# Kernel tuning notes

Hardware: AMD Instinct MI355X
Metric: run time of the kernel (lower is better)

Reference implementation:

```python
import jax, jax.numpy as jnp
import numpy as np


def setup_inputs() -> dict:
    key = jax.random.key(0)
    ks = jax.random.split(key, 5)
    N, D, H, E = 8192, 1024, 4096, 8
    s = 0.02
    return {
        "x": jax.random.normal(ks[0], (N, D), jnp.float32),
        "Wr": jax.random.normal(ks[1], (D, E), jnp.float32) * s,
        "br": jnp.zeros((E,), jnp.float32),
        "W1": jax.random.normal(ks[2], (E, D, H), jnp.float32) * s,
        "b1": jnp.zeros((E, H), jnp.float32),
        "W2": jax.random.normal(ks[3], (E, H, D), jnp.float32) * s,
        "b2": jnp.zeros((E, D), jnp.float32),
        "k": 2,
    }


def reference(x, Wr, br, W1, b1, W2, b2, k):
    # Router (eval mode: no gate noise)
    logits = x @ Wr + br                      # [N, E]
    scores = jax.nn.softmax(logits, axis=-1)  # [N, E]
    topk_vals, topk_inds = jax.lax.top_k(scores, k)  # [N, k]
    N, E = scores.shape
    # dispatch_mask: zeros scattered with top-k probabilities
    dispatch_mask = jnp.zeros_like(scores).at[
        jnp.arange(N)[:, None], topk_inds
    ].set(topk_vals)                          # [N, E]
    # Dense all-expert FFN compute (faithful to the original wasteful pattern)
    h = jax.nn.relu(jnp.einsum('nd,edh->neh', x, W1) + b1)   # [N, E, H]
    expert_outputs = jnp.einsum('neh,ehd->ned', h, W2) + b2  # [N, E, D]
    output = jnp.einsum('ned,ne->nd', expert_outputs, dispatch_mask)  # [N, D]
    # Load-balancing aux loss (torch.var is unbiased, ddof=1)
    importance = dispatch_mask.sum(axis=0)    # [E]
    imp_mean = jnp.mean(importance)
    imp_var = jnp.var(importance, ddof=1)
    aux_loss = imp_var / (imp_mean ** 2 + 1e-9)
    return output, aux_loss
```

## Files before the change

kernel.cpp:

```cpp
#include <hip/hip_runtime.h>
#include <hip/hip_bf16.h>


#define NTOK 8192
#define DDIM 1024
#define HDIM 4096
#define NEXP 8
#define NASSIGN (NTOK * 2)
#define MAX_MTILES 136

typedef __bf16 bf16_t;
typedef __bf16 bf16x8 __attribute__((ext_vector_type(8)));
typedef float f32x4 __attribute__((ext_vector_type(4)));

#define GLOAD16(gptr, lptr)                                                    \
  __builtin_amdgcn_global_load_lds(                                            \
      (const __attribute__((address_space(1))) void*)(gptr),                   \
      (__attribute__((address_space(3))) void*)(lptr), 16, 0, 0)


__global__ void __launch_bounds__(256) cvt_x_kernel(
    const float* __restrict__ in, bf16_t* __restrict__ out) {
  const int i = (blockIdx.x * 256 + threadIdx.x) * 8;
  const float4 a = *(const float4*)(in + i);
  const float4 b = *(const float4*)(in + i + 4);
  bf16x8 o;
  o[0] = (bf16_t)a.x; o[1] = (bf16_t)a.y; o[2] = (bf16_t)a.z; o[3] = (bf16_t)a.w;
  o[4] = (bf16_t)b.x; o[5] = (bf16_t)b.y; o[6] = (bf16_t)b.z; o[7] = (bf16_t)b.w;
  *(bf16x8*)(out + i) = o;
}

__global__ void __launch_bounds__(256) transpose_cvt_kernel(
    const float* __restrict__ in, bf16_t* __restrict__ out, int R, int C) {
  __shared__ float tile[32][33];
  const size_t mat = (size_t)R * C;
  const float* ip = in + (size_t)blockIdx.z * mat;
  bf16_t* op = out + (size_t)blockIdx.z * mat;
  const int c0 = blockIdx.x * 32, r0 = blockIdx.y * 32;
  const int tx = threadIdx.x, ty = threadIdx.y;
#pragma unroll
  for (int i = 0; i < 4; ++i) {
    const int r = ty + 8 * i;
    tile[r][tx] = ip[(size_t)(r0 + r) * C + (c0 + tx)];
  }
  __syncthreads();
#pragma unroll
  for (int i = 0; i < 4; ++i) {
    const int r = ty + 8 * i;
    op[(size_t)(c0 + r) * R + (r0 + tx)] = (bf16_t)tile[tx][r];
  }
}


__global__ void __launch_bounds__(256) router_kernel(
    const float* __restrict__ x, const float* __restrict__ Wr,
    const float* __restrict__ br, int2* __restrict__ ids,
    float2* __restrict__ prs, int* __restrict__ counts) {
  const int n = blockIdx.x;
  const int t = threadIdx.x;
  const float* xr = x + (size_t)n * DDIM;
  float acc[NEXP];
#pragma unroll
  for (int e = 0; e < NEXP; ++e) acc[e] = 0.f;
#pragma unroll
  for (int j = 0; j < DDIM / 256; ++j) {
    const int d = t + 256 * j;
    const float xv = xr[d];
    const float* w = Wr + (size_t)d * NEXP;
#pragma unroll
    for (int e = 0; e < NEXP; ++e) acc[e] += xv * w[e];
  }
  __shared__ float red[256][NEXP];
#pragma unroll
  for (int e = 0; e < NEXP; ++e) red[t][e] = acc[e];
  __syncthreads();
  for (int s = 128; s >= 1; s >>= 1) {
    if (t < s) {
#pragma unroll
      for (int e = 0; e < NEXP; ++e) red[t][e] += red[t + s][e];
    }
    __syncthreads();
  }
  if (t == 0) {
    float l[NEXP];
#pragma unroll
    for (int e = 0; e < NEXP; ++e) l[e] = red[0][e] + br[e];
    int i1 = 0; float v1 = l[0];
    for (int e = 1; e < NEXP; ++e)
      if (l[e] > v1) { v1 = l[e]; i1 = e; }
    int i2 = (i1 == 0) ? 1 : 0; float v2 = l[i2];
    for (int e = 0; e < NEXP; ++e)
      if (e != i1 && l[e] > v2) { v2 = l[e]; i2 = e; }
    float denom = 0.f;
    for (int e = 0; e < NEXP; ++e) denom += expf(l[e] - v1);
    const float p1 = expf(v1 - v1) / denom;
    const float p2 = expf(v2 - v1) / denom;
    ids[n] = make_int2(i1, i2);
    prs[n] = make_float2(p1, p2);
    atomicAdd(&counts[i1], 1);
    atomicAdd(&counts[i2], 1);
  }
}

__global__ void scan_kernel(const int* __restrict__ counts,
                            int* __restrict__ offsets, int* __restrict__ tmap) {
  if (threadIdx.x != 0 || blockIdx.x != 0) return;
  int off = 0, nt = 0;
  for (int e = 0; e < NEXP; ++e) {
    offsets[e] = off;
    const int c = counts[e];
    for (int m0 = 0; m0 < c; m0 += 128) {
      tmap[nt] = e;
      tmap[MAX_MTILES + nt] = m0;
      ++nt;
    }
    off += c;
  }
  offsets[NEXP] = off;
  tmap[2 * MAX_MTILES] = nt;
}

__global__ void __launch_bounds__(256) scatter_kernel(
    const int2* __restrict__ ids, const float2* __restrict__ prs,
    const int* __restrict__ offsets, int* __restrict__ cursor,
    int* __restrict__ btok, float* __restrict__ bprob) {
  const int n = blockIdx.x * 256 + threadIdx.x;
  if (n >= NTOK) return;
  const int2 id = ids[n];
  const float2 pr = prs[n];
  int p = atomicAdd(&cursor[id.x], 1);
  btok[offsets[id.x] + p] = n;
  bprob[offsets[id.x] + p] = pr.x;
  p = atomicAdd(&cursor[id.y], 1);
  btok[offsets[id.y] + p] = n;
  bprob[offsets[id.y] + p] = pr.y;
}

__global__ void __launch_bounds__(256) aux_kernel(
    const int2* __restrict__ ids, const float2* __restrict__ prs,
    float* __restrict__ aux_out) {
  const int t = threadIdx.x;
  float imp[NEXP];
#pragma unroll
  for (int e = 0; e < NEXP; ++e) imp[e] = 0.f;
  for (int n = t; n < NTOK; n += 256) {
    const int2 id = ids[n];
    const float2 pr = prs[n];
#pragma unroll
    for (int e = 0; e < NEXP; ++e)
      imp[e] += (id.x == e ? pr.x : 0.f) + (id.y == e ? pr.y : 0.f);
  }
  __shared__ float red[256][NEXP];
#pragma unroll
  for (int e = 0; e < NEXP; ++e) red[t][e] = imp[e];
  __syncthreads();
  for (int s = 128; s >= 1; s >>= 1) {
    if (t < s) {
#pragma unroll
      for (int e = 0; e < NEXP; ++e) red[t][e] += red[t + s][e];
    }
    __syncthreads();
  }
  if (t == 0) {
    float m = 0.f;
    for (int e = 0; e < NEXP; ++e) m += red[0][e];
    m *= (1.f / NEXP);
    float v = 0.f;
    for (int e = 0; e < NEXP; ++e) {
      const float d = red[0][e] - m;
      v += d * d;
    }
    v *= (1.f / (NEXP - 1));
    aux_out[0] = v / (m * m + 1e-9f);
  }
}


__global__ void __launch_bounds__(256) gemm1_kernel(
    const bf16_t* __restrict__ xb, const bf16_t* __restrict__ W1t,
    const float* __restrict__ b1, const int* __restrict__ btok,
    const int* __restrict__ offsets, const int* __restrict__ counts,
    const int* __restrict__ tmap, bf16_t* __restrict__ h) {
  const int tidx = blockIdx.y;
  if (tidx >= tmap[2 * MAX_MTILES]) return;
  const int e = tmap[tidx];
  const int m0 = tmap[MAX_MTILES + tidx];
  const int cnt = counts[e];
  const int aoff = offsets[e];
  const int n0 = blockIdx.x * 128;

  __shared__ __align__(16) bf16_t Al[128 * 32];
  __shared__ __align__(16) bf16_t Bl[128 * 32];

  const int tid = threadIdx.x;
  const int wave = tid >> 6;
  const int lane = tid & 63;

  const bf16_t* asrc[2];
  const bf16_t* bsrc[2];
#pragma unroll
  for (int j = 0; j < 2; ++j) {
    const int fi = j * 256 + tid;
    const int r = fi >> 2;
    const int kc = (fi & 3) * 8;
    int arow = m0 + r;
    if (arow > cnt - 1) arow = cnt - 1;
    const int tok = btok[aoff + arow];
    asrc[j] = xb + (size_t)tok * DDIM + kc;
    bsrc[j] = W1t + ((size_t)e * HDIM + n0 + r) * DDIM + kc;
  }
  char* AlB = (char*)Al + wave * 1024;
  char* BlB = (char*)Bl + wave * 1024;

  f32x4 acc[4][4];
#pragma unroll
  for (int mt = 0; mt < 4; ++mt)
#pragma unroll
    for (int nt = 0; nt < 4; ++nt) acc[mt][nt] = (f32x4){0.f, 0.f, 0.f, 0.f};

  const int wr = (wave >> 1) * 64;
  const int wc = (wave & 1) * 64;
  const int lrow = lane & 15;
  const int lk = (lane >> 4) * 8;

  for (int k0 = 0; k0 < DDIM; k0 += 32) {
    GLOAD16(asrc[0] + k0, AlB);
    GLOAD16(asrc[1] + k0, AlB + 4096);
    GLOAD16(bsrc[0] + k0, BlB);
    GLOAD16(bsrc[1] + k0, BlB + 4096);
    __syncthreads();
    bf16x8 af[4], bfr[4];
#pragma unroll
    for (int mt = 0; mt < 4; ++mt)
      af[mt] = *(const bf16x8*)&Al[(wr + mt * 16 + lrow) * 32 + lk];
#pragma unroll
    for (int nt = 0; nt < 4; ++nt)
      bfr[nt] = *(const bf16x8*)&Bl[(wc + nt * 16 + lrow) * 32 + lk];
#pragma unroll
    for (int mt = 0; mt < 4; ++mt)
#pragma unroll
      for (int nt = 0; nt < 4; ++nt)
        acc[mt][nt] = __builtin_amdgcn_mfma_f32_16x16x32_bf16(
            af[mt], bfr[nt], acc[mt][nt], 0, 0, 0);
    __syncthreads();
  }

  const int rbase = (lane >> 4) * 4;
  const float* b1e = b1 + (size_t)e * HDIM + n0;
#pragma unroll
  for (int nt = 0; nt < 4; ++nt) {
    const int cl = wc + nt * 16 + lrow;
    const float bb = b1e[cl];
#pragma unroll
    for (int mt = 0; mt < 4; ++mt) {
#pragma unroll
      for (int r = 0; r < 4; ++r) {
        const int grow = wr + mt * 16 + rbase + r;
        if (m0 + grow < cnt)
          h[(size_t)(aoff + m0 + grow) * HDIM + (n0 + cl)] =
              (bf16_t)fmaxf(acc[mt][nt][r] + bb, 0.f);
      }
    }
  }
}

__global__ void __launch_bounds__(256) gemm2_kernel(
    const bf16_t* __restrict__ h, const bf16_t* __restrict__ W2t,
    const float* __restrict__ b2, const int* __restrict__ btok,
    const float* __restrict__ bprob, const int* __restrict__ offsets,
    const int* __restrict__ counts, const int* __restrict__ tmap,
    float* __restrict__ out) {
  const int tidx = blockIdx.y;
  if (tidx >= tmap[2 * MAX_MTILES]) return;
  const int e = tmap[tidx];
  const int m0 = tmap[MAX_MTILES + tidx];
  const int cnt = counts[e];
  const int aoff = offsets[e];
  const int n0 = blockIdx.x * 128;

  __shared__ __align__(16) bf16_t Al[128 * 32];
  __shared__ __align__(16) bf16_t Bl[128 * 32];

  const int tid = threadIdx.x;
  const int wave = tid >> 6;
  const int lane = tid & 63;

  const bf16_t* asrc[2];
  const bf16_t* bsrc[2];
#pragma unroll
  for (int j = 0; j < 2; ++j) {
    const int fi = j * 256 + tid;
    const int r = fi >> 2;
    const int kc = (fi & 3) * 8;
    int arow = m0 + r;
    if (arow > cnt - 1) arow = cnt - 1;
    asrc[j] = h + (size_t)(aoff + arow) * HDIM + kc;
    bsrc[j] = W2t + ((size_t)e * DDIM + n0 + r) * HDIM + kc;
  }
  char* AlB = (char*)Al + wave * 1024;
  char* BlB = (char*)Bl + wave * 1024;

  f32x4 acc[4][4];
#pragma unroll
  for (int mt = 0; mt < 4; ++mt)
#pragma unroll
    for (int nt = 0; nt < 4; ++nt) acc[mt][nt] = (f32x4){0.f, 0.f, 0.f, 0.f};

  const int wr = (wave >> 1) * 64;
  const int wc = (wave & 1) * 64;
  const int lrow = lane & 15;
  const int lk = (lane >> 4) * 8;

  for (int k0 = 0; k0 < HDIM; k0 += 32) {
    GLOAD16(asrc[0] + k0, AlB);
    GLOAD16(asrc[1] + k0, AlB + 4096);
    GLOAD16(bsrc[0] + k0, BlB);
    GLOAD16(bsrc[1] + k0, BlB + 4096);
    __syncthreads();
    bf16x8 af[4], bfr[4];
#pragma unroll
    for (int mt = 0; mt < 4; ++mt)
      af[mt] = *(const bf16x8*)&Al[(wr + mt * 16 + lrow) * 32 + lk];
#pragma unroll
    for (int nt = 0; nt < 4; ++nt)
      bfr[nt] = *(const bf16x8*)&Bl[(wc + nt * 16 + lrow) * 32 + lk];
#pragma unroll
    for (int mt = 0; mt < 4; ++mt)
#pragma unroll
      for (int nt = 0; nt < 4; ++nt)
        acc[mt][nt] = __builtin_amdgcn_mfma_f32_16x16x32_bf16(
            af[mt], bfr[nt], acc[mt][nt], 0, 0, 0);
    __syncthreads();
  }

  const int rbase = (lane >> 4) * 4;
  const float* b2e = b2 + (size_t)e * DDIM + n0;
  float bb[4];
#pragma unroll
  for (int nt = 0; nt < 4; ++nt) bb[nt] = b2e[wc + nt * 16 + lrow];
#pragma unroll
  for (int mt = 0; mt < 4; ++mt) {
#pragma unroll
    for (int r = 0; r < 4; ++r) {
      const int grow = wr + mt * 16 + rbase + r;
      if (m0 + grow < cnt) {
        const int assign = aoff + m0 + grow;
        const int tok = btok[assign];
        const float p = bprob[assign];
        float* orow = out + (size_t)tok * DDIM + n0;
#pragma unroll
        for (int nt = 0; nt < 4; ++nt) {
          const int cl = wc + nt * 16 + lrow;
          atomicAdd(&orow[cl], (acc[mt][nt][r] + bb[nt]) * p);
        }
      }
    }
  }
}


extern "C" void kernel_launch(void* const* d_in, const int* in_sizes, int n_in,
                              void* d_out, int out_size, void* d_ws,
                              size_t ws_size, hipStream_t stream) {
  const float* x = (const float*)d_in[0];
  const float* Wr = (const float*)d_in[1];
  const float* br = (const float*)d_in[2];
  const float* W1 = (const float*)d_in[3];
  const float* b1 = (const float*)d_in[4];
  const float* W2 = (const float*)d_in[5];
  const float* b2 = (const float*)d_in[6];

  char* w = (char*)d_ws;
  auto alloc = [&](size_t bytes) -> char* {
    char* p = w;
    w += (bytes + 255) & ~(size_t)255;
    return p;
  };
  bf16_t* xb = (bf16_t*)alloc((size_t)NTOK * DDIM * 2);
  bf16_t* W1t = (bf16_t*)alloc((size_t)NEXP * DDIM * HDIM * 2);
  bf16_t* W2t = (bf16_t*)alloc((size_t)NEXP * DDIM * HDIM * 2);
  bf16_t* hbuf = (bf16_t*)alloc((size_t)NASSIGN * HDIM * 2);
  int* btok = (int*)alloc(NASSIGN * 4);
  float* bprob = (float*)alloc(NASSIGN * 4);
  int2* ids = (int2*)alloc(NTOK * 8);
  float2* prs = (float2*)alloc(NTOK * 8);
  int* ctrl = (int*)alloc(64);
  int* offsets = (int*)alloc(64);
  int* tmap = (int*)alloc((2 * MAX_MTILES + 1) * 4);
  int* counts = ctrl;
  int* cursor = ctrl + 8;
  (void)in_sizes; (void)n_in; (void)ws_size;

  float* out = (float*)d_out;

  hipMemsetAsync(d_out, 0, (size_t)out_size * 4, stream);
  hipMemsetAsync(ctrl, 0, 64, stream);

  cvt_x_kernel<<<NTOK * DDIM / 2048, 256, 0, stream>>>(x, xb);
  transpose_cvt_kernel<<<dim3(HDIM / 32, DDIM / 32, NEXP), dim3(32, 8), 0,
                         stream>>>(W1, W1t, DDIM, HDIM);
  transpose_cvt_kernel<<<dim3(DDIM / 32, HDIM / 32, NEXP), dim3(32, 8), 0,
                         stream>>>(W2, W2t, HDIM, DDIM);
  router_kernel<<<NTOK, 256, 0, stream>>>(x, Wr, br, ids, prs, counts);
  scan_kernel<<<1, 1, 0, stream>>>(counts, offsets, tmap);
  scatter_kernel<<<NTOK / 256, 256, 0, stream>>>(ids, prs, offsets, cursor,
                                                 btok, bprob);
  aux_kernel<<<1, 256, 0, stream>>>(ids, prs, out + (size_t)NTOK * DDIM);
  gemm1_kernel<<<dim3(HDIM / 128, MAX_MTILES - 1, 1), 256, 0, stream>>>(
      xb, W1t, b1, btok, offsets, counts, tmap, hbuf);
  gemm2_kernel<<<dim3(DDIM / 128, MAX_MTILES - 1, 1), 256, 0, stream>>>(
      hbuf, W2t, b2, btok, bprob, offsets, counts, tmap, out);
}
```

Measured before the change: 887.5 us.

## Enlarge grouped GEMM tiles to 256x256 with 512 threads and merge scan/aux kernels

Both expert GEMMs move from 128x128 tiles on 256 threads to 256x256 tiles on 512 threads. Each wave now computes a 128x64 sub-tile with 8x4 MFMA accumulators, and the LDS buffers double in size. M-tiles per expert are now 256 rows, so the tile map shrinks and the grid holds fewer, larger blocks. This raises arithmetic intensity per loaded byte, but it costs register pressure, more padding waste on the last partial tile of each expert, and fewer blocks to fill the CUs. The scan and aux-loss kernels are also merged into one launch.

```diff
diff --git a/kernel.cpp b/kernel.cpp
--- a/kernel.cpp
+++ b/kernel.cpp
@@ -7,7 +7,7 @@
 #define HDIM 4096
 #define NEXP 8
 #define NASSIGN (NTOK * 2)
-#define MAX_MTILES 136
+#define MAX_MT 72
 
 typedef __bf16 bf16_t;
 typedef __bf16 bf16x8 __attribute__((ext_vector_type(8)));
@@ -102,22 +102,59 @@
   }
 }
 
-__global__ void scan_kernel(const int* __restrict__ counts,
-                            int* __restrict__ offsets, int* __restrict__ tmap) {
-  if (threadIdx.x != 0 || blockIdx.x != 0) return;
-  int off = 0, nt = 0;
-  for (int e = 0; e < NEXP; ++e) {
-    offsets[e] = off;
-    const int c = counts[e];
-    for (int m0 = 0; m0 < c; m0 += 128) {
-      tmap[nt] = e;
-      tmap[MAX_MTILES + nt] = m0;
-      ++nt;
-    }
-    off += c;
-  }
-  offsets[NEXP] = off;
-  tmap[2 * MAX_MTILES] = nt;
+__global__ void __launch_bounds__(256) scan_aux_kernel(
+    const int* __restrict__ counts, int* __restrict__ offsets,
+    int* __restrict__ tmap, const int2* __restrict__ ids,
+    const float2* __restrict__ prs, float* __restrict__ aux_out) {
+  const int t = threadIdx.x;
+  if (t == 0) {
+    int off = 0, nt = 0;
+    for (int e = 0; e < NEXP; ++e) {
+      offsets[e] = off;
+      const int c = counts[e];
+      for (int m0 = 0; m0 < c; m0 += 256) {
+        tmap[nt] = e;
+        tmap[MAX_MT + nt] = m0;
+        ++nt;
+      }
+      off += c;
+    }
+    offsets[NEXP] = off;
+    tmap[2 * MAX_MT] = nt;
+  }
+  float imp[NEXP];
+#pragma unroll
+  for (int e = 0; e < NEXP; ++e) imp[e] = 0.f;
+  for (int n = t; n < NTOK; n += 256) {
+    const int2 id = ids[n];
+    const float2 pr = prs[n];
+#pragma unroll
+    for (int e = 0; e < NEXP; ++e)
+      imp[e] += (id.x == e ? pr.x : 0.f) + (id.y == e ? pr.y : 0.f);
+  }
+  __shared__ float red[256][NEXP];
+#pragma unroll
+  for (int e = 0; e < NEXP; ++e) red[t][e] = imp[e];
+  __syncthreads();
+  for (int s = 128; s >= 1; s >>= 1) {
+    if (t < s) {
+#pragma unroll
+      for (int e = 0; e < NEXP; ++e) red[t][e] += red[t + s][e];
+    }
+    __syncthreads();
+  }
+  if (t == 0) {
+    float m = 0.f;
+    for (int e = 0; e < NEXP; ++e) m += red[0][e];
+    m *= (1.f / NEXP);
+    float v = 0.f;
+    for (int e = 0; e < NEXP; ++e) {
+      const float d = red[0][e] - m;
+      v += d * d;
+    }
+    v *= (1.f / (NEXP - 1));
+    aux_out[0] = v / (m * m + 1e-9f);
+  }
 }
 
 __global__ void __launch_bounds__(256) scatter_kernel(
@@ -136,61 +173,22 @@
   bprob[offsets[id.y] + p] = pr.y;
 }
 
-__global__ void __launch_bounds__(256) aux_kernel(
-    const int2* __restrict__ ids, const float2* __restrict__ prs,
-    float* __restrict__ aux_out) {
-  const int t = threadIdx.x;
-  float imp[NEXP];
-#pragma unroll
-  for (int e = 0; e < NEXP; ++e) imp[e] = 0.f;
-  for (int n = t; n < NTOK; n += 256) {
-    const int2 id = ids[n];
-    const float2 pr = prs[n];
-#pragma unroll
-    for (int e = 0; e < NEXP; ++e)
-      imp[e] += (id.x == e ? pr.x : 0.f) + (id.y == e ? pr.y : 0.f);
-  }
-  __shared__ float red[256][NEXP];
-#pragma unroll
-  for (int e = 0; e < NEXP; ++e) red[t][e] = imp[e];
-  __syncthreads();
-  for (int s = 128; s >= 1; s >>= 1) {
-    if (t < s) {
-#pragma unroll
-      for (int e = 0; e < NEXP; ++e) red[t][e] += red[t + s][e];
-    }
-    __syncthreads();
-  }
-  if (t == 0) {
-    float m = 0.f;
-    for (int e = 0; e < NEXP; ++e) m += red[0][e];
-    m *= (1.f / NEXP);
-    float v = 0.f;
-    for (int e = 0; e < NEXP; ++e) {
-      const float d = red[0][e] - m;
-      v += d * d;
-    }
-    v *= (1.f / (NEXP - 1));
-    aux_out[0] = v / (m * m + 1e-9f);
-  }
-}
-
-
-__global__ void __launch_bounds__(256) gemm1_kernel(
+
+__global__ void __launch_bounds__(512, 2) gemm1_kernel(
     const bf16_t* __restrict__ xb, const bf16_t* __restrict__ W1t,
     const float* __restrict__ b1, const int* __restrict__ btok,
     const int* __restrict__ offsets, const int* __restrict__ counts,
     const int* __restrict__ tmap, bf16_t* __restrict__ h) {
   const int tidx = blockIdx.y;
-  if (tidx >= tmap[2 * MAX_MTILES]) return;
+  if (tidx >= tmap[2 * MAX_MT]) return;
   const int e = tmap[tidx];
-  const int m0 = tmap[MAX_MTILES + tidx];
+  const int m0 = tmap[MAX_MT + tidx];
   const int cnt = counts[e];
   const int aoff = offsets[e];
-  const int n0 = blockIdx.x * 128;
-
-  __shared__ __align__(16) bf16_t Al[128 * 32];
-  __shared__ __align__(16) bf16_t Bl[128 * 32];
+  const int n0 = blockIdx.x * 256;
+
+  __shared__ __align__(16) bf16_t Al[256 * 32];
+  __shared__ __align__(16) bf16_t Bl[256 * 32];
 
   const int tid = threadIdx.x;
   const int wave = tid >> 6;
@@ -200,9 +198,9 @@
   const bf16_t* bsrc[2];
 #pragma unroll
   for (int j = 0; j < 2; ++j) {
-    const int fi = j * 256 + tid;
-    const int r = fi >> 2;
-    const int kc = (fi & 3) * 8;
+    const int c = j * 512 + tid;
+    const int r = c >> 2;
+    const int kc = (c & 3) * 8;
     int arow = m0 + r;
     if (arow > cnt - 1) arow = cnt - 1;
     const int tok = btok[aoff + arow];
@@ -212,74 +210,74 @@
   char* AlB = (char*)Al + wave * 1024;
   char* BlB = (char*)Bl + wave * 1024;
 
-  f32x4 acc[4][4];
-#pragma unroll
-  for (int mt = 0; mt < 4; ++mt)
-#pragma unroll
-    for (int nt = 0; nt < 4; ++nt) acc[mt][nt] = (f32x4){0.f, 0.f, 0.f, 0.f};
-
-  const int wr = (wave >> 1) * 64;
-  const int wc = (wave & 1) * 64;
+  f32x4 acc[8][4];
+#pragma unroll
+  for (int mf = 0; mf < 8; ++mf)
+#pragma unroll
+    for (int nf = 0; nf < 4; ++nf) acc[mf][nf] = (f32x4){0.f, 0.f, 0.f, 0.f};
+
+  const int wr = (wave >> 2) * 128;
+  const int wc = (wave & 3) * 64;
   const int lrow = lane & 15;
   const int lk = (lane >> 4) * 8;
 
   for (int k0 = 0; k0 < DDIM; k0 += 32) {
     GLOAD16(asrc[0] + k0, AlB);
-    GLOAD16(asrc[1] + k0, AlB + 4096);
+    GLOAD16(asrc[1] + k0, AlB + 8192);
     GLOAD16(bsrc[0] + k0, BlB);
-    GLOAD16(bsrc[1] + k0, BlB + 4096);
-    __syncthreads();
-    bf16x8 af[4], bfr[4];
-#pragma unroll
-    for (int mt = 0; mt < 4; ++mt)
-      af[mt] = *(const bf16x8*)&Al[(wr + mt * 16 + lrow) * 32 + lk];
-#pragma unroll
-    for (int nt = 0; nt < 4; ++nt)
-      bfr[nt] = *(const bf16x8*)&Bl[(wc + nt * 16 + lrow) * 32 + lk];
-#pragma unroll
-    for (int mt = 0; mt < 4; ++mt)
-#pragma unroll
-      for (int nt = 0; nt < 4; ++nt)
-        acc[mt][nt] = __builtin_amdgcn_mfma_f32_16x16x32_bf16(
-            af[mt], bfr[nt], acc[mt][nt], 0, 0, 0);
+    GLOAD16(bsrc[1] + k0, BlB + 8192);
+    __syncthreads();
+    bf16x8 af[8], bfr[4];
+#pragma unroll
+    for (int mf = 0; mf < 8; ++mf)
+      af[mf] = *(const bf16x8*)&Al[(wr + mf * 16 + lrow) * 32 + lk];
+#pragma unroll
+    for (int nf = 0; nf < 4; ++nf)
+      bfr[nf] = *(const bf16x8*)&Bl[(wc + nf * 16 + lrow) * 32 + lk];
+#pragma unroll
+    for (int mf = 0; mf < 8; ++mf)
+#pragma unroll
+      for (int nf = 0; nf < 4; ++nf)
+        acc[mf][nf] = __builtin_amdgcn_mfma_f32_16x16x32_bf16(
+            af[mf], bfr[nf], acc[mf][nf], 0, 0, 0);
     __syncthreads();
   }
 
   const int rbase = (lane >> 4) * 4;
   const float* b1e = b1 + (size_t)e * HDIM + n0;
 #pragma unroll
-  for (int nt = 0; nt < 4; ++nt) {
-    const int cl = wc + nt * 16 + lrow;
+  for (int nf = 0; nf < 4; ++nf) {
+    const int cl = wc + nf * 16 + lrow;
     const float bb = b1e[cl];
 #pragma unroll
-    for (int mt = 0; mt < 4; ++mt) {
+    for (int mf = 0; mf < 8; ++mf) {
 #pragma unroll
       for (int r = 0; r < 4; ++r) {
-        const int grow = wr + mt * 16 + rbase + r;
+        const int grow = wr + mf * 16 + rbase + r;
         if (m0 + grow < cnt)
           h[(size_t)(aoff + m0 + grow) * HDIM + (n0 + cl)] =
-              (bf16_t)fmaxf(acc[mt][nt][r] + bb, 0.f);
+              (bf16_t)fmaxf(acc[mf][nf][r] + bb, 0.f);
       }
     }
   }
 }
 
-__global__ void __launch_bounds__(256) gemm2_kernel(
+__global__ void __launch_bounds__(512, 2) gemm2_kernel(
     const bf16_t* __restrict__ h, const bf16_t* __restrict__ W2t,
     const float* __restrict__ b2, const int* __restrict__ btok,
     const float* __restrict__ bprob, const int* __restrict__ offsets,
     const int* __restrict__ counts, const int* __restrict__ tmap,
     float* __restrict__ out) {
   const int tidx = blockIdx.y;
-  if (tidx >= tmap[2 * MAX_MTILES]) return;
+  if (tidx >= tmap[2 * MAX_MT]) return;
   const int e = tmap[tidx];
-  const int m0 = tmap[MAX_MTILES + tidx];
+  const int m0 = tmap[MAX_MT + tidx];
   const int cnt = counts[e];
   const int aoff = offsets[e];
-  const int n0 = blockIdx.x * 128;
-
-  __shared__ __align__(16) bf16_t Al[128 * 32];
-  __shared__ __align__(16) bf16_t Bl[128 * 32];
+  const int n0 = blockIdx.x * 256;
+
+  __shared__ __align__(16) bf16_t Al[256 * 32];
+  __shared__ __align__(16) bf16_t Bl[256 * 32];
 
   const int tid = threadIdx.x;
   const int wave = tid >> 6;
@@ -289,9 +287,9 @@
   const bf16_t* bsrc[2];
 #pragma unroll
   for (int j = 0; j < 2; ++j) {
-    const int fi = j * 256 + tid;
-    const int r = fi >> 2;
-    const int kc = (fi & 3) * 8;
+    const int c = j * 512 + tid;
+    const int r = c >> 2;
+    const int kc = (c & 3) * 8;
     int arow = m0 + r;
     if (arow > cnt - 1) arow = cnt - 1;
     asrc[j] = h + (size_t)(aoff + arow) * HDIM + kc;
@@ -300,36 +298,36 @@
   char* AlB = (char*)Al + wave * 1024;
   char* BlB = (char*)Bl + wave * 1024;
 
-  f32x4 acc[4][4];
-#pragma unroll
-  for (int mt = 0; mt < 4; ++mt)
-#pragma unroll
-    for (int nt = 0; nt < 4; ++nt) acc[mt][nt] = (f32x4){0.f, 0.f, 0.f, 0.f};
-
-  const int wr = (wave >> 1) * 64;
-  const int wc = (wave & 1) * 64;
+  f32x4 acc[8][4];
+#pragma unroll
+  for (int mf = 0; mf < 8; ++mf)
+#pragma unroll
+    for (int nf = 0; nf < 4; ++nf) acc[mf][nf] = (f32x4){0.f, 0.f, 0.f, 0.f};
+
+  const int wr = (wave >> 2) * 128;
+  const int wc = (wave & 3) * 64;
   const int lrow = lane & 15;
   const int lk = (lane >> 4) * 8;
 
   for (int k0 = 0; k0 < HDIM; k0 += 32) {
     GLOAD16(asrc[0] + k0, AlB);
-    GLOAD16(asrc[1] + k0, AlB + 4096);
+    GLOAD16(asrc[1] + k0, AlB + 8192);
     GLOAD16(bsrc[0] + k0, BlB);
-    GLOAD16(bsrc[1] + k0, BlB + 4096);
-    __syncthreads();
-    bf16x8 af[4], bfr[4];
-#pragma unroll
-    for (int mt = 0; mt < 4; ++mt)
-      af[mt] = *(const bf16x8*)&Al[(wr + mt * 16 + lrow) * 32 + lk];
-#pragma unroll
-    for (int nt = 0; nt < 4; ++nt)
-      bfr[nt] = *(const bf16x8*)&Bl[(wc + nt * 16 + lrow) * 32 + lk];
-#pragma unroll
-    for (int mt = 0; mt < 4; ++mt)
-#pragma unroll
-      for (int nt = 0; nt < 4; ++nt)
-        acc[mt][nt] = __builtin_amdgcn_mfma_f32_16x16x32_bf16(
-            af[mt], bfr[nt], acc[mt][nt], 0, 0, 0);
+    GLOAD16(bsrc[1] + k0, BlB + 8192);
+    __syncthreads();
+    bf16x8 af[8], bfr[4];
+#pragma unroll
+    for (int mf = 0; mf < 8; ++mf)
+      af[mf] = *(const bf16x8*)&Al[(wr + mf * 16 + lrow) * 32 + lk];
+#pragma unroll
+    for (int nf = 0; nf < 4; ++nf)
+      bfr[nf] = *(const bf16x8*)&Bl[(wc + nf * 16 + lrow) * 32 + lk];
+#pragma unroll
+    for (int mf = 0; mf < 8; ++mf)
+#pragma unroll
+      for (int nf = 0; nf < 4; ++nf)
+        acc[mf][nf] = __builtin_amdgcn_mfma_f32_16x16x32_bf16(
+            af[mf], bfr[nf], acc[mf][nf], 0, 0, 0);
     __syncthreads();
   }
 
@@ -337,21 +335,21 @@
   const float* b2e = b2 + (size_t)e * DDIM + n0;
   float bb[4];
 #pragma unroll
-  for (int nt = 0; nt < 4; ++nt) bb[nt] = b2e[wc + nt * 16 + lrow];
-#pragma unroll
-  for (int mt = 0; mt < 4; ++mt) {
+  for (int nf = 0; nf < 4; ++nf) bb[nf] = b2e[wc + nf * 16 + lrow];
+#pragma unroll
+  for (int mf = 0; mf < 8; ++mf) {
 #pragma unroll
     for (int r = 0; r < 4; ++r) {
-      const int grow = wr + mt * 16 + rbase + r;
+      const int grow = wr + mf * 16 + rbase + r;
       if (m0 + grow < cnt) {
         const int assign = aoff + m0 + grow;
         const int tok = btok[assign];
         const float p = bprob[assign];
         float* orow = out + (size_t)tok * DDIM + n0;
 #pragma unroll
-        for (int nt = 0; nt < 4; ++nt) {
-          const int cl = wc + nt * 16 + lrow;
-          atomicAdd(&orow[cl], (acc[mt][nt][r] + bb[nt]) * p);
+        for (int nf = 0; nf < 4; ++nf) {
+          const int cl = wc + nf * 16 + lrow;
+          atomicAdd(&orow[cl], (acc[mf][nf][r] + bb[nf]) * p);
         }
       }
     }
@@ -386,7 +384,7 @@
   float2* prs = (float2*)alloc(NTOK * 8);
   int* ctrl = (int*)alloc(64);
   int* offsets = (int*)alloc(64);
-  int* tmap = (int*)alloc((2 * MAX_MTILES + 1) * 4);
+  int* tmap = (int*)alloc((2 * MAX_MT + 1) * 4);
   int* counts = ctrl;
   int* cursor = ctrl + 8;
   (void)in_sizes; (void)n_in; (void)ws_size;
@@ -402,12 +400,12 @@
   transpose_cvt_kernel<<<dim3(DDIM / 32, HDIM / 32, NEXP), dim3(32, 8), 0,
                          stream>>>(W2, W2t, HDIM, DDIM);
   router_kernel<<<NTOK, 256, 0, stream>>>(x, Wr, br, ids, prs, counts);
-  scan_kernel<<<1, 1, 0, stream>>>(counts, offsets, tmap);
+  scan_aux_kernel<<<1, 256, 0, stream>>>(counts, offsets, tmap, ids, prs,
+                                         out + (size_t)NTOK * DDIM);
   scatter_kernel<<<NTOK / 256, 256, 0, stream>>>(ids, prs, offsets, cursor,
                                                  btok, bprob);
-  aux_kernel<<<1, 256, 0, stream>>>(ids, prs, out + (size_t)NTOK * DDIM);
-  gemm1_kernel<<<dim3(HDIM / 128, MAX_MTILES - 1, 1), 256, 0, stream>>>(
+  gemm1_kernel<<<dim3(HDIM / 256, MAX_MT, 1), 512, 0, stream>>>(
       xb, W1t, b1, btok, offsets, counts, tmap, hbuf);
-  gemm2_kernel<<<dim3(DDIM / 128, MAX_MTILES - 1, 1), 256, 0, stream>>>(
+  gemm2_kernel<<<dim3(DDIM / 256, MAX_MT, 1), 512, 0, stream>>>(
       hbuf, W2t, b2, btok, bprob, offsets, counts, tmap, out);
 }
```

Result: slower. 1.020 ms (+14.9%).
